# Kernel optimization log

Measured on AMD Instinct MI355X. Metric: run time of the kernel, lower is better.

Reference implementation:

```python
import jax, jax.numpy as jnp
import numpy as np

B, NP, FEAT = 128, 196, 2048
E = 512   # embed_dim
D = 512   # decoder_dim == attention_dim (required by the source: h1 = att1(feats_mean))
V = 10000 # vocab
L = 52    # max caption length -> T = 51 decode steps


def setup_inputs() -> dict:
    key = jax.random.key(0)
    ks = jax.random.split(key, 12)
    image_features = jax.random.normal(ks[0], (B, NP, FEAT), dtype=jnp.float32)
    encoded_captions = jax.random.randint(ks[1], (B, L), 0, V)
    caption_lengths = jax.random.randint(ks[2], (B, 1), 2, L + 1)
    # force max decode length == L-1 so predictions has a static shape matching torch's max(decode_lengths)
    caption_lengths = caption_lengths.at[0, 0].set(L)
    u = lambda k, s, a: jax.random.uniform(k, s, jnp.float32, -a, a)
    emb_table = u(ks[3], (V, E), 0.1)          # embedding.weight.uniform_(-0.1, 0.1)
    att1_w = u(ks[4], (D, FEAT), 1.0 / np.sqrt(FEAT))
    att1_b = u(ks[5], (D,), 1.0 / np.sqrt(FEAT))
    kd = 1.0 / np.sqrt(D)
    w_ih = u(ks[6], (4 * D, E), kd)
    w_hh = u(ks[7], (4 * D, D), kd)
    b_ih = u(ks[8], (4 * D,), kd)
    b_hh = u(ks[9], (4 * D,), kd)
    word_w = u(ks[10], (V, D), 0.1)            # word.weight.uniform_(-0.1, 0.1)
    word_b = jnp.zeros((V,), jnp.float32)      # word.bias.fill_(0)
    return {"image_features": image_features, "encoded_captions": encoded_captions,
            "caption_lengths": caption_lengths, "emb_table": emb_table,
            "att1_w": att1_w, "att1_b": att1_b, "w_ih": w_ih, "w_hh": w_hh,
            "b_ih": b_ih, "b_hh": b_hh, "word_w": word_w, "word_b": word_b}


def reference(image_features, encoded_captions, caption_lengths, emb_table,
              att1_w, att1_b, w_ih, w_hh, b_ih, b_hh, word_w, word_b):
    lens = caption_lengths[:, 0]
    sort_ind = jnp.argsort(-lens)                      # descending (stable)
    lens_s = lens[sort_ind]
    feats_mean = jnp.mean(image_features, axis=1)[sort_ind]   # [B, FEAT]
    caps = encoded_captions[sort_ind]                  # [B, L]
    emb = emb_table[caps]                              # [B, L, E]
    h0 = feats_mean @ att1_w.T + att1_b               # h1 = att1(mean feats); needs attention_dim == decoder_dim
    c0 = jnp.zeros_like(h0)
    dec_len = lens_s - 1                               # decode_lengths
    T = caps.shape[1] - 1
    # active mask: row b participates at step t iff dec_len[b] > t (rows sorted descending)
    mask = (jnp.arange(T)[None, :] < dec_len[:, None])  # [B, T] bool

    def step(carry, xs):
        h, c = carry
        x_t, m_t = xs                                   # [B,E], [B]
        gates = x_t @ w_ih.T + b_ih + h @ w_hh.T + b_hh  # [B, 4D]
        i, f, g, o = jnp.split(gates, 4, axis=-1)
        i = jax.nn.sigmoid(i); f = jax.nn.sigmoid(f)
        g = jnp.tanh(g);       o = jax.nn.sigmoid(o)
        c_new = f * c + i * g
        h_new = o * jnp.tanh(c_new)
        m = m_t[:, None]
        h2 = jnp.where(m, h_new, h)                     # inactive rows keep frozen state
        c2 = jnp.where(m, c_new, c)
        # dropout is identity in eval mode; inactive rows stay zero (predictions init)
        pred = (h_new @ word_w.T + word_b) * m          # [B, V]
        return (h2, c2), pred

    xs = (jnp.swapaxes(emb[:, :T, :], 0, 1), mask.T)    # time-major
    _, preds = jax.lax.scan(step, (h0, c0), xs)         # [T, B, V]
    predictions = jnp.swapaxes(preds, 0, 1)             # [B, T, V]
    return predictions, caps, dec_len, sort_ind
```

## Files before the change

### kernel.cpp

```cpp
#include <hip/hip_runtime.h>


typedef __attribute__((ext_vector_type(8))) short bf16x8;
typedef __attribute__((ext_vector_type(4))) float f32x4;

#define B_ 128
#define T_ 51
#define D_ 512
#define V_ 10000
#define FEAT_ 2048
#define NROW (T_ * B_)
#define PRED_ELEMS (B_ * T_ * V_)

#define HBF_OFF    0
#define C_OFF      6815744
#define XMEAN_OFF  7077888
#define CAPST_OFF  7602176
#define NB_OFF     7628288
#define SORT_OFF   7628544
#define SMALL_END  7629056
#define WORDBF_OFF 7629056
#define WHHBF_OFF  17869056
#define BIG_END    19966208

__device__ __forceinline__ float b2f(unsigned short u) {
    union { unsigned int i; float f; } v; v.i = ((unsigned int)u) << 16; return v.f;
}
__device__ __forceinline__ unsigned short f2b(float f) {
    union { float f; unsigned int i; } v; v.f = f;
    unsigned int r = v.i + 0x7FFFu + ((v.i >> 16) & 1u);
    return (unsigned short)(r >> 16);
}
__device__ __forceinline__ float sigmoid_(float x) { return 1.0f / (1.0f + __expf(-x)); }
__device__ __forceinline__ float tanh_(float x) {
    float ax = fabsf(x);
    float e = __expf(-2.0f * ax);
    float r = (1.0f - e) / (1.0f + e);
    return copysignf(r, x);
}

__device__ __forceinline__ bf16x8 ldfrag(const unsigned short* p) {
    return *(const bf16x8*)p;
}
__device__ __forceinline__ bf16x8 ldfrag(const float* p) {
    f32x4 a = *(const f32x4*)p;
    f32x4 b = *(const f32x4*)(p + 4);
    bf16x8 r;
#pragma unroll
    for (int j = 0; j < 4; ++j) { r[j] = (short)f2b(a[j]); r[j + 4] = (short)f2b(b[j]); }
    return r;
}

__global__ void prep_kernel(const int* __restrict__ caplen,
                            const int* __restrict__ caps_in,
                            int* __restrict__ capsT, int* __restrict__ nb,
                            int* __restrict__ sortind,
                            float* __restrict__ out_caps,
                            float* __restrict__ out_declen,
                            float* __restrict__ out_sortind) {
    __shared__ int s_len[B_], s_sort[B_], s_lens_s[B_];
    int b = threadIdx.x;
    int li = caplen[b];
    s_len[b] = li;
    __syncthreads();
    int rank = 0;
    for (int j = 0; j < B_; ++j) {
        int lj = s_len[j];
        rank += (lj > li) || (lj == li && j < b);
    }
    s_sort[rank] = b;
    __syncthreads();
    int ob = s_sort[b];
    sortind[b] = ob;
    out_sortind[b] = (float)ob;
    int ls = s_len[ob];
    s_lens_s[b] = ls;
    out_declen[b] = (float)(ls - 1);
    for (int l = 0; l < 52; ++l) {
        int tok = caps_in[ob * 52 + l];
        out_caps[b * 52 + l] = (float)tok;
        if (l < T_) capsT[l * B_ + b] = tok;
    }
    __syncthreads();
    if (b < T_) {
        int cnt = 0;
        for (int j = 0; j < B_; ++j) cnt += (s_lens_s[j] - 1 > b) ? 1 : 0;
        nb[b] = cnt;
    }
}

__global__ void cast8_kernel(const float* __restrict__ src,
                             unsigned short* __restrict__ dst, int n8) {
    int i = blockIdx.x * blockDim.x + threadIdx.x;
    if (i >= n8) return;
    *(bf16x8*)(dst + (size_t)i * 8) = ldfrag(src + (size_t)i * 8);
}

__global__ void feats_mean_kernel(const float* __restrict__ feats,
                                  const int* __restrict__ sortind,
                                  unsigned short* __restrict__ xmean) {
    int bs = blockIdx.x;
    int ob = sortind[bs];
    int c8 = blockIdx.y * 1024 + threadIdx.x * 8;
    const float* base = feats + (size_t)ob * 196 * FEAT_ + c8;
    float acc[8];
#pragma unroll
    for (int j = 0; j < 8; ++j) acc[j] = 0.f;
    for (int p = 0; p < 196; ++p) {
        f32x4 a = *(const f32x4*)(base + (size_t)p * FEAT_);
        f32x4 b = *(const f32x4*)(base + (size_t)p * FEAT_ + 4);
#pragma unroll
        for (int j = 0; j < 4; ++j) { acc[j] += a[j]; acc[j + 4] += b[j]; }
    }
    const float inv = 1.0f / 196.0f;
    bf16x8 o;
#pragma unroll
    for (int j = 0; j < 8; ++j) o[j] = (short)f2b(acc[j] * inv);
    *(bf16x8*)(xmean + bs * FEAT_ + c8) = o;
}

__global__ void __launch_bounds__(256) h0_kernel(
    const unsigned short* __restrict__ xmean,
    const float* __restrict__ att1_w,
    const float* __restrict__ att1_b,
    unsigned short* __restrict__ hbf0) {
    int lane = threadIdx.x & 63;
    int gw = blockIdx.x * 4 + (threadIdx.x >> 6);
    int m0 = (gw >> 5) * 16;
    int n0 = (gw & 31) * 16;
    int kbase = (lane >> 4) * 8;
    const unsigned short* Ap = xmean + (m0 + (lane & 15)) * FEAT_ + kbase;
    const float* Bp = att1_w + (size_t)(n0 + (lane & 15)) * FEAT_ + kbase;
    f32x4 acc = {0.f, 0.f, 0.f, 0.f};
    for (int k = 0; k < FEAT_ / 32; ++k) {
        bf16x8 a = ldfrag(Ap + k * 32);
        bf16x8 b = ldfrag(Bp + k * 32);
        acc = __builtin_amdgcn_mfma_f32_16x16x32_bf16(a, b, acc, 0, 0, 0);
    }
    int n = n0 + (lane & 15);
    float bias = att1_b[n];
    int rbase = m0 + (lane >> 4) * 4;
#pragma unroll
    for (int r = 0; r < 4; ++r) hbf0[(rbase + r) * D_ + n] = f2b(acc[r] + bias);
}

__global__ void __launch_bounds__(256) xgates_kernel(
    const float* __restrict__ emb,
    const float* __restrict__ w_ih,
    const float* __restrict__ b_ih,
    const float* __restrict__ b_hh,
    const int* __restrict__ capsT, const int* __restrict__ nb,
    unsigned short* __restrict__ xg) {
    int r0 = blockIdx.x * 64;
    int t = r0 >> 7;
    int b0 = r0 & 127;
    if (b0 >= nb[t]) return;
    int lane = threadIdx.x & 63;
    int w = threadIdx.x >> 6;
    int c0 = blockIdx.y * 256 + w * 64;
    int kbase = (lane >> 4) * 8;
    int nlo = lane & 15;
    const float* Ap[4];
    const float* Bp[4];
#pragma unroll
    for (int i = 0; i < 4; ++i) {
        int tok = capsT[r0 + i * 16 + nlo];
        Ap[i] = emb + (size_t)tok * D_ + kbase;
        Bp[i] = w_ih + (size_t)(c0 + i * 16 + nlo) * D_ + kbase;
    }
    f32x4 acc[4][4];
#pragma unroll
    for (int i = 0; i < 4; ++i)
#pragma unroll
        for (int j = 0; j < 4; ++j) acc[i][j] = (f32x4){0.f, 0.f, 0.f, 0.f};
    for (int k = 0; k < D_ / 32; ++k) {
        bf16x8 a[4], bb[4];
#pragma unroll
        for (int i = 0; i < 4; ++i) a[i] = ldfrag(Ap[i] + k * 32);
#pragma unroll
        for (int i = 0; i < 4; ++i) bb[i] = ldfrag(Bp[i] + k * 32);
#pragma unroll
        for (int im = 0; im < 4; ++im)
#pragma unroll
            for (int in = 0; in < 4; ++in)
                acc[im][in] = __builtin_amdgcn_mfma_f32_16x16x32_bf16(a[im], bb[in], acc[im][in], 0, 0, 0);
    }
    int qr = (lane >> 4) * 4;
#pragma unroll
    for (int in = 0; in < 4; ++in) {
        int n = c0 + in * 16 + nlo;
        float bias = b_ih[n] + b_hh[n];
#pragma unroll
        for (int im = 0; im < 4; ++im)
#pragma unroll
            for (int rr = 0; rr < 4; ++rr) {
                int r = r0 + im * 16 + qr + rr;
                xg[(size_t)r * 2048 + n] = f2b(acc[im][in][rr] + bias);
            }
    }
}

template <typename TB>
__global__ void __launch_bounds__(256) chain_kernel(
    const TB* __restrict__ w_hh,
    const unsigned short* __restrict__ xg,
    unsigned short* __restrict__ hbf, float* __restrict__ cst, int t) {
    int lane = threadIdx.x & 63;
    int gw = blockIdx.x * 4 + (threadIdx.x >> 6);
    int m0 = (gw >> 5) * 16;
    int n0 = (gw & 31) * 16;
    const unsigned short* hin = hbf + (size_t)t * (B_ * D_);
    unsigned short* hout = hbf + (size_t)(t + 1) * (B_ * D_);
    int kbase = (lane >> 4) * 8;
    int nlo = lane & 15;
    const unsigned short* Ap = hin + (m0 + nlo) * D_ + kbase;
    const TB* Bp[4];
#pragma unroll
    for (int g = 0; g < 4; ++g)
        Bp[g] = w_hh + (size_t)(g * D_ + n0 + nlo) * D_ + kbase;
    f32x4 acc[4];
#pragma unroll
    for (int g = 0; g < 4; ++g) acc[g] = (f32x4){0.f, 0.f, 0.f, 0.f};
    for (int k = 0; k < D_ / 32; ++k) {
        bf16x8 a = ldfrag(Ap + k * 32);
#pragma unroll
        for (int g = 0; g < 4; ++g) {
            bf16x8 b = ldfrag(Bp[g] + k * 32);
            acc[g] = __builtin_amdgcn_mfma_f32_16x16x32_bf16(a, b, acc[g], 0, 0, 0);
        }
    }
    int n = n0 + nlo;
    int qr = (lane >> 4) * 4;
    const unsigned short* xgr = xg + (size_t)t * B_ * 2048;
#pragma unroll
    for (int rr = 0; rr < 4; ++rr) {
        int m = m0 + qr + rr;
        const unsigned short* xrow = xgr + (size_t)m * 2048;
        float iv = sigmoid_(acc[0][rr] + b2f(xrow[n]));
        float fv = sigmoid_(acc[1][rr] + b2f(xrow[D_ + n]));
        float gv = tanh_(acc[2][rr] + b2f(xrow[2 * D_ + n]));
        float ov = sigmoid_(acc[3][rr] + b2f(xrow[3 * D_ + n]));
        float co = cst[m * D_ + n];
        float cn = fv * co + iv * gv;
        cst[m * D_ + n] = cn;
        hout[m * D_ + n] = f2b(ov * tanh_(cn));
    }
}

template <typename TB>
__global__ void __launch_bounds__(256) pred_kernel(
    const unsigned short* __restrict__ hbf,
    const TB* __restrict__ word_w,
    const float* __restrict__ word_b,
    const int* __restrict__ nb, float* __restrict__ out) {
    int lane = threadIdx.x & 63;
    int w = threadIdx.x >> 6;
    int r0 = blockIdx.x * 64;
    int t = r0 >> 7;
    int b0 = r0 & 127;
    int c0 = blockIdx.y * 256 + w * 64;
    int nbt = nb[t];
    if (b0 >= nbt) {
        int cc = c0 + lane;
        if (cc < V_) {
            for (int rr = 0; rr < 64; ++rr)
                out[(size_t)(b0 + rr) * (T_ * V_) + (size_t)t * V_ + cc] = 0.f;
        }
        return;
    }
    int kbase = (lane >> 4) * 8;
    int nlo = lane & 15;
    const unsigned short* hrow = hbf + (size_t)(t + 1) * (B_ * D_);
    const unsigned short* Ap[4];
    const TB* Bp[4];
    int cvalid[4];
#pragma unroll
    for (int i = 0; i < 4; ++i) {
        Ap[i] = hrow + (size_t)(b0 + i * 16 + nlo) * D_ + kbase;
        int c = c0 + i * 16 + nlo;
        cvalid[i] = (c0 + i * 16) < V_;
        int cc = c < V_ ? c : (V_ - 1);
        Bp[i] = word_w + (size_t)cc * D_ + kbase;
    }
    f32x4 acc[4][4];
#pragma unroll
    for (int i = 0; i < 4; ++i)
#pragma unroll
        for (int j = 0; j < 4; ++j) acc[i][j] = (f32x4){0.f, 0.f, 0.f, 0.f};
    for (int k = 0; k < D_ / 32; ++k) {
        bf16x8 a[4], bb[4];
#pragma unroll
        for (int i = 0; i < 4; ++i) a[i] = ldfrag(Ap[i] + k * 32);
#pragma unroll
        for (int i = 0; i < 4; ++i) bb[i] = ldfrag(Bp[i] + k * 32);
#pragma unroll
        for (int im = 0; im < 4; ++im)
#pragma unroll
            for (int in = 0; in < 4; ++in)
                acc[im][in] = __builtin_amdgcn_mfma_f32_16x16x32_bf16(a[im], bb[in], acc[im][in], 0, 0, 0);
    }
    int qr = (lane >> 4) * 4;
#pragma unroll
    for (int in = 0; in < 4; ++in) {
        if (!cvalid[in]) continue;
        int c = c0 + in * 16 + nlo;
        float wb = word_b[c];
#pragma unroll
        for (int im = 0; im < 4; ++im)
#pragma unroll
            for (int rr = 0; rr < 4; ++rr) {
                int brow = b0 + im * 16 + qr + rr;
                float v = (brow < nbt) ? (acc[im][in][rr] + wb) : 0.0f;
                out[(size_t)brow * (T_ * V_) + (size_t)t * V_ + c] = v;
            }
    }
}

extern "C" void kernel_launch(void* const* d_in, const int* in_sizes, int n_in,
                              void* d_out, int out_size, void* d_ws, size_t ws_size,
                              hipStream_t stream) {
    const float* feats = (const float*)d_in[0];
    const int* caps_in = (const int*)d_in[1];
    const int* caplen = (const int*)d_in[2];
    const float* emb = (const float*)d_in[3];
    const float* att1_w = (const float*)d_in[4];
    const float* att1_b = (const float*)d_in[5];
    const float* w_ih = (const float*)d_in[6];
    const float* w_hh = (const float*)d_in[7];
    const float* b_ih = (const float*)d_in[8];
    const float* b_hh = (const float*)d_in[9];
    const float* word_w = (const float*)d_in[10];
    const float* word_b = (const float*)d_in[11];
    float* out = (float*)d_out;
    (void)in_sizes; (void)n_in; (void)out_size;

    char* ws = (char*)d_ws;
    unsigned short* hbf = (unsigned short*)(ws + HBF_OFF);
    float* cst = (float*)(ws + C_OFF);
    unsigned short* xmean = (unsigned short*)(ws + XMEAN_OFF);
    int* capsT = (int*)(ws + CAPST_OFF);
    int* nb = (int*)(ws + NB_OFF);
    int* sortind = (int*)(ws + SORT_OFF);
    unsigned short* wordbf = (unsigned short*)(ws + WORDBF_OFF);
    unsigned short* whhbf = (unsigned short*)(ws + WHHBF_OFF);
    const bool big = ws_size >= (size_t)BIG_END;

    unsigned short* xg = (unsigned short*)d_out;

    float* out_caps = out + PRED_ELEMS;
    float* out_declen = out_caps + B_ * 52;
    float* out_sortind = out_declen + B_;

    hipMemsetAsync(cst, 0, B_ * D_ * sizeof(float), stream);
    prep_kernel<<<1, 128, 0, stream>>>(caplen, caps_in, capsT, nb, sortind,
                                       out_caps, out_declen, out_sortind);
    feats_mean_kernel<<<dim3(128, 2), 128, 0, stream>>>(feats, sortind, xmean);
    h0_kernel<<<64, 256, 0, stream>>>(xmean, att1_w, att1_b, hbf);
    if (big) {
        cast8_kernel<<<(640000 + 255) / 256, 256, 0, stream>>>(word_w, wordbf, 640000);
        cast8_kernel<<<(131072 + 255) / 256, 256, 0, stream>>>(w_hh, whhbf, 131072);
    }
    xgates_kernel<<<dim3(102, 8), 256, 0, stream>>>(emb, w_ih, b_ih, b_hh, capsT, nb, xg);
    if (big) {
        for (int t = 0; t < T_; ++t)
            chain_kernel<unsigned short><<<64, 256, 0, stream>>>(whhbf, xg, hbf, cst, t);
        pred_kernel<unsigned short><<<dim3(102, 40), 256, 0, stream>>>(hbf, wordbf, word_b, nb, out);
    } else {
        for (int t = 0; t < T_; ++t)
            chain_kernel<float><<<64, 256, 0, stream>>>(w_hh, xg, hbf, cst, t);
        pred_kernel<float><<<dim3(102, 40), 256, 0, stream>>>(hbf, word_w, word_b, nb, out);
    }
}
```

Baseline: 1.441 ms.

## Fuse per-step LSTM chain launches into one persistent kernel with grid barrier

Replaces 51 separate chain kernel launches with a single persistent kernel that loops over time steps and synchronises all 64 blocks through an atomic counter barrier in workspace. The cell state now lives in registers instead of a global buffer, which removes its per-step load and store. The aim is to cut launch overhead and inter-kernel gaps on the serial recurrence. In exchange it relies on all 64 blocks being co-resident, and the spin barrier adds its own latency.

```diff
diff --git a/kernel.cpp b/kernel.cpp
--- a/kernel.cpp
+++ b/kernel.cpp
@@ -13,7 +13,7 @@
 #define PRED_ELEMS (B_ * T_ * V_)
 
 #define HBF_OFF    0
-#define C_OFF      6815744
+#define BAR_OFF    6815744
 #define XMEAN_OFF  7077888
 #define CAPST_OFF  7602176
 #define NB_OFF     7628288
@@ -201,49 +201,64 @@
 }
 
 template <typename TB>
-__global__ void __launch_bounds__(256) chain_kernel(
+__global__ void __launch_bounds__(256) chain_persist_kernel(
     const TB* __restrict__ w_hh,
     const unsigned short* __restrict__ xg,
-    unsigned short* __restrict__ hbf, float* __restrict__ cst, int t) {
+    unsigned short* __restrict__ hbf,
+    int* __restrict__ bar) {
     int lane = threadIdx.x & 63;
     int gw = blockIdx.x * 4 + (threadIdx.x >> 6);
     int m0 = (gw >> 5) * 16;
     int n0 = (gw & 31) * 16;
-    const unsigned short* hin = hbf + (size_t)t * (B_ * D_);
-    unsigned short* hout = hbf + (size_t)(t + 1) * (B_ * D_);
     int kbase = (lane >> 4) * 8;
     int nlo = lane & 15;
-    const unsigned short* Ap = hin + (m0 + nlo) * D_ + kbase;
+    int qr = (lane >> 4) * 4;
+    int n = n0 + nlo;
     const TB* Bp[4];
 #pragma unroll
     for (int g = 0; g < 4; ++g)
         Bp[g] = w_hh + (size_t)(g * D_ + n0 + nlo) * D_ + kbase;
-    f32x4 acc[4];
-#pragma unroll
-    for (int g = 0; g < 4; ++g) acc[g] = (f32x4){0.f, 0.f, 0.f, 0.f};
-    for (int k = 0; k < D_ / 32; ++k) {
-        bf16x8 a = ldfrag(Ap + k * 32);
-#pragma unroll
-        for (int g = 0; g < 4; ++g) {
-            bf16x8 b = ldfrag(Bp[g] + k * 32);
-            acc[g] = __builtin_amdgcn_mfma_f32_16x16x32_bf16(a, b, acc[g], 0, 0, 0);
+    float creg[4] = {0.f, 0.f, 0.f, 0.f};
+
+    for (int t = 0; t < T_; ++t) {
+        const unsigned short* hin = hbf + (size_t)t * (B_ * D_);
+        unsigned short* hout = hbf + (size_t)(t + 1) * (B_ * D_);
+        const unsigned short* Ap = hin + (m0 + nlo) * D_ + kbase;
+        f32x4 acc[4];
+#pragma unroll
+        for (int g = 0; g < 4; ++g) acc[g] = (f32x4){0.f, 0.f, 0.f, 0.f};
+        for (int k = 0; k < D_ / 32; ++k) {
+            bf16x8 a = ldfrag(Ap + k * 32);
+#pragma unroll
+            for (int g = 0; g < 4; ++g) {
+                bf16x8 b = ldfrag(Bp[g] + k * 32);
+                acc[g] = __builtin_amdgcn_mfma_f32_16x16x32_bf16(a, b, acc[g], 0, 0, 0);
+            }
         }
-    }
-    int n = n0 + nlo;
-    int qr = (lane >> 4) * 4;
-    const unsigned short* xgr = xg + (size_t)t * B_ * 2048;
-#pragma unroll
-    for (int rr = 0; rr < 4; ++rr) {
-        int m = m0 + qr + rr;
-        const unsigned short* xrow = xgr + (size_t)m * 2048;
-        float iv = sigmoid_(acc[0][rr] + b2f(xrow[n]));
-        float fv = sigmoid_(acc[1][rr] + b2f(xrow[D_ + n]));
-        float gv = tanh_(acc[2][rr] + b2f(xrow[2 * D_ + n]));
-        float ov = sigmoid_(acc[3][rr] + b2f(xrow[3 * D_ + n]));
-        float co = cst[m * D_ + n];
-        float cn = fv * co + iv * gv;
-        cst[m * D_ + n] = cn;
-        hout[m * D_ + n] = f2b(ov * tanh_(cn));
+        const unsigned short* xgr = xg + (size_t)t * B_ * 2048;
+#pragma unroll
+        for (int rr = 0; rr < 4; ++rr) {
+            int m = m0 + qr + rr;
+            const unsigned short* xrow = xgr + (size_t)m * 2048;
+            float iv = sigmoid_(acc[0][rr] + b2f(xrow[n]));
+            float fv = sigmoid_(acc[1][rr] + b2f(xrow[D_ + n]));
+            float gv = tanh_(acc[2][rr] + b2f(xrow[2 * D_ + n]));
+            float ov = sigmoid_(acc[3][rr] + b2f(xrow[3 * D_ + n]));
+            float cn = fv * creg[rr] + iv * gv;
+            creg[rr] = cn;
+            hout[m * D_ + n] = f2b(ov * tanh_(cn));
+        }
+        __threadfence();
+        __syncthreads();
+        if (threadIdx.x == 0) {
+            __hip_atomic_fetch_add(bar, 1, __ATOMIC_RELEASE, __HIP_MEMORY_SCOPE_AGENT);
+            int target = (t + 1) * (int)gridDim.x;
+            while (__hip_atomic_load(bar, __ATOMIC_ACQUIRE, __HIP_MEMORY_SCOPE_AGENT) < target) {
+                __builtin_amdgcn_s_sleep(1);
+            }
+        }
+        __syncthreads();
+        __threadfence();
     }
 }
 
@@ -336,7 +351,7 @@
 
     char* ws = (char*)d_ws;
     unsigned short* hbf = (unsigned short*)(ws + HBF_OFF);
-    float* cst = (float*)(ws + C_OFF);
+    int* bar = (int*)(ws + BAR_OFF);
     unsigned short* xmean = (unsigned short*)(ws + XMEAN_OFF);
     int* capsT = (int*)(ws + CAPST_OFF);
     int* nb = (int*)(ws + NB_OFF);
@@ -351,7 +366,7 @@
     float* out_declen = out_caps + B_ * 52;
     float* out_sortind = out_declen + B_;
 
-    hipMemsetAsync(cst, 0, B_ * D_ * sizeof(float), stream);
+    hipMemsetAsync(bar, 0, 64, stream);
     prep_kernel<<<1, 128, 0, stream>>>(caplen, caps_in, capsT, nb, sortind,
                                        out_caps, out_declen, out_sortind);
     feats_mean_kernel<<<dim3(128, 2), 128, 0, stream>>>(feats, sortind, xmean);
@@ -362,12 +377,10 @@
     }
     xgates_kernel<<<dim3(102, 8), 256, 0, stream>>>(emb, w_ih, b_ih, b_hh, capsT, nb, xg);
     if (big) {
-        for (int t = 0; t < T_; ++t)
-            chain_kernel<unsigned short><<<64, 256, 0, stream>>>(whhbf, xg, hbf, cst, t);
+        chain_persist_kernel<unsigned short><<<64, 256, 0, stream>>>(whhbf, xg, hbf, bar);
         pred_kernel<unsigned short><<<dim3(102, 40), 256, 0, stream>>>(hbf, wordbf, word_b, nb, out);
     } else {
-        for (int t = 0; t < T_; ++t)
-            chain_kernel<float><<<64, 256, 0, stream>>>(w_hh, xg, hbf, cst, t);
+        chain_persist_kernel<float><<<64, 256, 0, stream>>>(w_hh, xg, hbf, bar);
         pred_kernel<float><<<dim3(102, 40), 256, 0, stream>>>(hbf, word_w, word_b, nb, out);
     }
 }
```

Result: slower. 1.871 ms (+29.9%).
